# Kernel tuning notes

Hardware: AMD Instinct MI355X
Metric: run time of the kernel (lower is better)

Reference implementation:

```python
import jax, jax.numpy as jnp
import numpy as np

NEG_SLOPE = 0.2
EPS = 1e-5

N_NODES = 50000
N_GRAPHS = 500
NODES_PER_GRAPH = 100
N_EDGES = 500000
F_IN = 16
F_GRAPH = 4
HID = 64
N_CLASSES = 2


def setup_inputs() -> dict:
    key = jax.random.key(0)
    ks = jax.random.split(key, 32)
    x = jax.random.normal(ks[0], (N_NODES, F_IN), dtype=jnp.float32)
    # intra-graph random edges: dst lives in the same 100-node block as src
    src = jax.random.randint(ks[1], (N_EDGES,), 0, N_NODES)
    dst = (src // NODES_PER_GRAPH) * NODES_PER_GRAPH + jax.random.randint(ks[2], (N_EDGES,), 0, NODES_PER_GRAPH)
    edge_index = jnp.stack([src, dst]).astype(jnp.int64)
    graph_input = jax.random.normal(ks[3], (N_GRAPHS, F_GRAPH), dtype=jnp.float32)
    batch = (jnp.arange(N_NODES) // NODES_PER_GRAPH).astype(jnp.int64)

    def w(k, shape, scale=0.1):
        return (jax.random.normal(k, shape, dtype=jnp.float32) * scale)

    inp = dict(x=x, edge_index=edge_index, graph_input=graph_input, batch=batch)
    # GraphNorm params
    inp['gn_w'] = jnp.ones((F_IN,), jnp.float32)
    inp['gn_b'] = w(ks[4], (F_IN,))
    inp['gn_ms'] = jnp.ones((F_IN,), jnp.float32)
    inp['W1'] = w(ks[5], (F_IN, 4 * HID))
    inp['as1'] = w(ks[6], (4, HID)); inp['ad1'] = w(ks[7], (4, HID))
    inp['b1'] = w(ks[8], (4 * HID,))
    inp['W2'] = w(ks[9], (4 * HID, 4 * HID))
    inp['as2'] = w(ks[10], (4, HID)); inp['ad2'] = w(ks[11], (4, HID))
    inp['b2'] = w(ks[12], (4 * HID,))
    inp['W3'] = w(ks[13], (4 * HID, HID))
    inp['as3'] = w(ks[14], (1, HID)); inp['ad3'] = w(ks[15], (1, HID))
    inp['b3'] = w(ks[16], (HID,))
    # BatchNorm1d (eval mode) over [HID + F_GRAPH]
    D = HID + F_GRAPH
    inp['bn_g'] = 1.0 + w(ks[17], (D,))
    inp['bn_b'] = w(ks[18], (D,))
    inp['bn_m'] = jnp.zeros((D,), jnp.float32)
    inp['bn_v'] = jnp.ones((D,), jnp.float32)
    # Dense head
    inp['Wd1'] = w(ks[19], (D, HID)); inp['bd1'] = w(ks[20], (HID,))
    inp['Wd2'] = w(ks[21], (HID, HID)); inp['bd2'] = w(ks[22], (HID,))
    inp['Wo'] = w(ks[23], (HID, N_CLASSES)); inp['bo'] = w(ks[24], (N_CLASSES,))
    return inp


def _segment_softmax(e, seg, n):
    m = jax.ops.segment_max(e, seg, num_segments=n)
    ex = jnp.exp(e - m[seg])
    s = jax.ops.segment_sum(ex, seg, num_segments=n)
    return ex / s[seg]


def _gat_conv(x, src, dst, W, att_src, att_dst, b):
    N = x.shape[0]
    H, C = att_src.shape
    loop = jnp.arange(N)
    src = jnp.concatenate([src, loop])  # PyG GATConv adds self-loops
    dst = jnp.concatenate([dst, loop])
    h = (x @ W).reshape(N, H, C)
    a_src = (h * att_src).sum(-1)  # [N,H]
    a_dst = (h * att_dst).sum(-1)
    e = jax.nn.leaky_relu(a_src[src] + a_dst[dst], NEG_SLOPE)  # [E,H]
    alpha = _segment_softmax(e, dst, N)
    out = jax.ops.segment_sum(h[src] * alpha[:, :, None], dst, num_segments=N)
    return out.reshape(N, H * C) + b


def _graph_norm(x, batch, n_graphs, w, b, ms):
    cnt = jax.ops.segment_sum(jnp.ones((x.shape[0],), x.dtype), batch, num_segments=n_graphs)[:, None]
    mean = jax.ops.segment_sum(x, batch, num_segments=n_graphs) / cnt
    out = x - mean[batch] * ms
    var = jax.ops.segment_sum(out * out, batch, num_segments=n_graphs) / cnt
    return w * out / jnp.sqrt(var[batch] + EPS) + b


def _global_mean_pool(x, batch, n_graphs):
    cnt = jax.ops.segment_sum(jnp.ones((x.shape[0],), x.dtype), batch, num_segments=n_graphs)[:, None]
    return jax.ops.segment_sum(x, batch, num_segments=n_graphs) / cnt


def reference(x, edge_index, graph_input, batch,
              gn_w, gn_b, gn_ms,
              W1, as1, ad1, b1,
              W2, as2, ad2, b2,
              W3, as3, ad3, b3,
              bn_g, bn_b, bn_m, bn_v,
              Wd1, bd1, Wd2, bd2, Wo, bo):
    src, dst = edge_index[0], edge_index[1]
    G = graph_input.shape[0]
    h = _graph_norm(x, batch, G, gn_w, gn_b, gn_ms)
    # dropout is a no-op in eval
    h = jax.nn.elu(_gat_conv(h, src, dst, W1, as1, ad1, b1))
    h = jax.nn.elu(_gat_conv(h, src, dst, W2, as2, ad2, b2))
    h = _gat_conv(h, src, dst, W3, as3, ad3, b3)
    g = _global_mean_pool(h, batch, G)
    g = jnp.concatenate([g, graph_input], axis=1)
    g = (g - bn_m) / jnp.sqrt(bn_v + EPS) * bn_g + bn_b  # BatchNorm1d eval
    g = jax.nn.selu(g @ Wd1 + bd1)
    g = jax.nn.selu(g @ Wd2 + bd2)
    g = g @ Wo + bo
    return jax.nn.softmax(g, axis=1)
```

## Files before the change

kernel.cpp:

```cpp
#include <hip/hip_runtime.h>
#include <math.h>

#define N_NODES 50000
#define N_ROWS_PAD 50048
#define N_GRAPHS 500
#define NPG 100
#define N_EDGES 500000
#define F_IN 16
#define HID 64
#define EW_CAP 1408

#define SELU_SCALE 1.0507009873554804934193349852946f
#define SELU_ALPHA 1.6732632423543772848170429916717f

typedef __attribute__((ext_vector_type(8))) short short8;
typedef __attribute__((ext_vector_type(8))) unsigned short ushort8;
typedef __attribute__((ext_vector_type(4))) float floatx4;

__device__ __forceinline__ float lrelu(float x){ return x > 0.f ? x : 0.2f * x; }
__device__ __forceinline__ float eluf(float x){ return x > 0.f ? x : expf(x) - 1.f; }
__device__ __forceinline__ float seluf(float x){
    return x > 0.f ? SELU_SCALE * x : SELU_SCALE * (SELU_ALPHA * (expf(x) - 1.f));
}
__device__ __forceinline__ unsigned short f2bf(float x){
    unsigned u = __float_as_uint(x);
    return (unsigned short)((u + 0x7FFFu + ((u >> 16) & 1u)) >> 16);
}
__device__ __forceinline__ float bf2f(unsigned short u){
    return __uint_as_float((unsigned)u << 16);
}
__device__ __forceinline__ float bf2f_lo(unsigned u){
    return __uint_as_float(u << 16);
}
__device__ __forceinline__ float bf2f_hi(unsigned u){
    return __uint_as_float(u & 0xFFFF0000u);
}

__global__ void k_count(const int* __restrict__ dst, int* __restrict__ counts){
    int e = blockIdx.x * 256 + threadIdx.x;
    if (e < N_EDGES) atomicAdd(&counts[dst[e]], 1);
}

__global__ void k_local_scan(const int* __restrict__ counts, int* __restrict__ local_off,
                             int* __restrict__ graph_tot){
    __shared__ int s[128];
    int g = blockIdx.x, t = threadIdx.x;
    int v = (t < NPG) ? counts[g * NPG + t] : 0;
    s[t] = v; __syncthreads();
    for (int o = 1; o < 128; o <<= 1){
        int x = (t >= o) ? s[t - o] : 0;
        __syncthreads();
        s[t] += x;
        __syncthreads();
    }
    if (t < NPG) local_off[g * NPG + t] = s[t] - v;
    if (t == 127) graph_tot[g] = s[127];
}

__global__ void k_graph_scan(const int* __restrict__ graph_tot, int* __restrict__ graph_base){
    __shared__ int s[512];
    int t = threadIdx.x;
    int v = (t < N_GRAPHS) ? graph_tot[t] : 0;
    s[t] = v; __syncthreads();
    for (int o = 1; o < 512; o <<= 1){
        int x = (t >= o) ? s[t - o] : 0;
        __syncthreads();
        s[t] += x;
        __syncthreads();
    }
    if (t < N_GRAPHS) graph_base[t] = s[t] - v;
}

__global__ void k_off(const int* __restrict__ local_off, const int* __restrict__ graph_base,
                      int* __restrict__ node_off, int* __restrict__ write_ptr){
    int n = blockIdx.x * 256 + threadIdx.x;
    if (n < N_NODES){
        int v = local_off[n] + graph_base[n / NPG];
        node_off[n] = v;
        write_ptr[n] = v;
    }
}

__global__ void k_scatter(const int* __restrict__ src, const int* __restrict__ dst,
                          int* __restrict__ write_ptr, int* __restrict__ csr){
    int e = blockIdx.x * 256 + threadIdx.x;
    if (e < N_EDGES){
        int d = dst[e];
        int pos = atomicAdd(&write_ptr[d], 1);
        csr[pos] = src[e];
    }
}

__global__ void k_gnorm(const float* __restrict__ x, const float* __restrict__ w,
                        const float* __restrict__ b, const float* __restrict__ ms,
                        float* __restrict__ y){
    __shared__ float sx[NPG * F_IN];
    __shared__ float red[16][16];
    __shared__ float meanS[16], varS[16];
    int g = blockIdx.x, t = threadIdx.x;
    for (int idx = t; idx < NPG * F_IN; idx += 256) sx[idx] = x[g * NPG * F_IN + idx];
    __syncthreads();
    int f = t & 15, grp = t >> 4;
    float p = 0.f;
    for (int i = grp; i < NPG; i += 16) p += sx[i * 16 + f];
    red[grp][f] = p; __syncthreads();
    if (t < 16){
        float s = 0.f;
        for (int i = 0; i < 16; i++) s += red[i][t];
        meanS[t] = s * (1.f / 100.f);
    }
    __syncthreads();
    float mm = meanS[f] * ms[f];
    p = 0.f;
    for (int i = grp; i < NPG; i += 16){ float v = sx[i * 16 + f] - mm; p += v * v; }
    red[grp][f] = p; __syncthreads();
    if (t < 16){
        float s = 0.f;
        for (int i = 0; i < 16; i++) s += red[i][t];
        varS[t] = s * (1.f / 100.f);
    }
    __syncthreads();
    for (int idx = t; idx < NPG * F_IN; idx += 256){
        int ff = idx & 15;
        float v = sx[idx] - meanS[ff] * ms[ff];
        y[g * NPG * F_IN + idx] = w[ff] * v * rsqrtf(varS[ff] + 1e-5f) + b[ff];
    }
}

__global__ void k_gemm_tiled(const float* __restrict__ X, const float* __restrict__ W,
                             float* __restrict__ Y, int N, int K, int OUT){
    __shared__ float As[16][68];
    __shared__ float Bs[16][68];
    int t = threadIdx.x;
    int r0 = blockIdx.y * 64;
    int c0 = blockIdx.x * 64;
    int tx = t & 15, ty = t >> 4;
    float acc[4][4];
    #pragma unroll
    for (int i = 0; i < 4; i++)
        #pragma unroll
        for (int j = 0; j < 4; j++) acc[i][j] = 0.f;

    int lk = t & 15;
    int lm0 = t >> 4;
    int ln = t & 63;
    int lkb = t >> 6;

    for (int kt = 0; kt < K; kt += 16){
        #pragma unroll
        for (int i = 0; i < 4; i++){
            int m = lm0 + i * 16;
            int row = r0 + m;
            As[lk][m] = (row < N) ? X[row * K + kt + lk] : 0.f;
        }
        #pragma unroll
        for (int i = 0; i < 4; i++){
            int k = lkb + i * 4;
            Bs[k][ln] = W[(kt + k) * OUT + c0 + ln];
        }
        __syncthreads();
        #pragma unroll
        for (int k = 0; k < 16; k++){
            float4 a = *(const float4*)&As[k][ty * 4];
            float4 b = *(const float4*)&Bs[k][tx * 4];
            float av[4] = {a.x, a.y, a.z, a.w};
            float bv[4] = {b.x, b.y, b.z, b.w};
            #pragma unroll
            for (int i = 0; i < 4; i++)
                #pragma unroll
                for (int j = 0; j < 4; j++) acc[i][j] += av[i] * bv[j];
        }
        __syncthreads();
    }
    #pragma unroll
    for (int i = 0; i < 4; i++){
        int row = r0 + ty * 4 + i;
        if (row < N){
            float4 v = make_float4(acc[i][0], acc[i][1], acc[i][2], acc[i][3]);
            *(float4*)&Y[row * OUT + c0 + tx * 4] = v;
        }
    }
}

__global__ void k_pack_w(const float* __restrict__ W, unsigned short* __restrict__ Wp,
                         int K, int OUT){
    int idx = blockIdx.x * 256 + threadIdx.x;
    if (idx >= K * OUT) return;
    int k = idx / OUT, n = idx - k * OUT;
    Wp[(((k >> 3) * OUT) + n) * 8 + (k & 7)] = f2bf(W[idx]);
}

__global__ void k_gemm_mfma(const unsigned short* __restrict__ Xb,
                            const unsigned short* __restrict__ Wp,
                            float* __restrict__ Y, int N, int K, int OUT){
    int t = threadIdx.x;
    int wave = t >> 6, lane = t & 63;
    int quad = lane >> 4, ln = lane & 15;
    int r0 = blockIdx.y * 64 + wave * 16;
    int c0 = blockIdx.x * 64;

    floatx4 acc[4];
    #pragma unroll
    for (int f = 0; f < 4; f++) acc[f] = (floatx4){0.f, 0.f, 0.f, 0.f};

    const unsigned short* aptr = Xb + (size_t)(r0 + ln) * K + quad * 8;
    for (int kt = 0; kt < K; kt += 32){
        short8 a = *(const short8*)(aptr + kt);
        int kc = (kt >> 3) + quad;
        #pragma unroll
        for (int f = 0; f < 4; f++){
            short8 b = *(const short8*)(Wp + ((size_t)kc * OUT + c0 + f * 16 + ln) * 8);
            acc[f] = __builtin_amdgcn_mfma_f32_16x16x32_bf16(a, b, acc[f], 0, 0, 0);
        }
    }
    int rowb = r0 + quad * 4;
    #pragma unroll
    for (int f = 0; f < 4; f++){
        int col = c0 + f * 16 + ln;
        #pragma unroll
        for (int rg = 0; rg < 4; rg++){
            int row = rowb + rg;
            if (row < N) Y[(size_t)row * OUT + col] = acc[f][rg];
        }
    }
}

__global__ void __launch_bounds__(512)
k_fused4(const float* __restrict__ h, const float* __restrict__ as,
         const float* __restrict__ ad, const float* __restrict__ bias,
         const int* __restrict__ csr, const int* __restrict__ noff,
         const int* __restrict__ cnt, unsigned short* __restrict__ out_bf){
    __shared__ __align__(16) unsigned short hl[NPG * 256];
    __shared__ __align__(16) unsigned int edl[EW_CAP][4];
    __shared__ __align__(16) float asrcl[NPG * 4], adstl[NPG * 4];
    __shared__ __align__(16) float wselfl[NPG * 4], rsuml[NPG * 4];
    __shared__ int offl[NPG], cntl[NPG];

    int g = blockIdx.x, t = threadIdx.x;
    int wave = t >> 6, lane = t & 63;
    int base = g * NPG;

    int ebeg = noff[base];
    int etot = noff[base + NPG - 1] + cnt[base + NPG - 1] - ebeg;
    int eln = etot < EW_CAP ? etot : EW_CAP;

    for (int i = t; i < NPG * 16; i += 512){
        int node = i >> 4, c4 = i & 15;
        const float* hr = h + (size_t)(base + node) * 256 + c4 * 4;
        float4 f0 = *(const float4*)(hr);
        float4 f1 = *(const float4*)(hr + 64);
        float4 f2 = *(const float4*)(hr + 128);
        float4 f3 = *(const float4*)(hr + 192);
        ushort8 lo, hi;
        lo[0] = f2bf(f0.x); lo[1] = f2bf(f1.x); lo[2] = f2bf(f2.x); lo[3] = f2bf(f3.x);
        lo[4] = f2bf(f0.y); lo[5] = f2bf(f1.y); lo[6] = f2bf(f2.y); lo[7] = f2bf(f3.y);
        hi[0] = f2bf(f0.z); hi[1] = f2bf(f1.z); hi[2] = f2bf(f2.z); hi[3] = f2bf(f3.z);
        hi[4] = f2bf(f0.w); hi[5] = f2bf(f1.w); hi[6] = f2bf(f2.w); hi[7] = f2bf(f3.w);
        *(ushort8*)&hl[node * 256 + c4 * 16]     = lo;
        *(ushort8*)&hl[node * 256 + c4 * 16 + 8] = hi;
    }
    for (int i = t; i < eln; i += 512) edl[i][2] = (unsigned)(csr[ebeg + i] - base);
    if (t < NPG){ offl[t] = noff[base + t]; cntl[t] = cnt[base + t]; }
    __syncthreads();

    {
        int cl = lane & 15, nsub = lane >> 4;
        float av[4][4], dv[4][4];
        #pragma unroll
        for (int hh = 0; hh < 4; hh++){
            float4 a4 = *(const float4*)&as[hh * 64 + cl * 4];
            float4 d4 = *(const float4*)&ad[hh * 64 + cl * 4];
            av[hh][0] = a4.x; av[hh][1] = a4.y; av[hh][2] = a4.z; av[hh][3] = a4.w;
            dv[hh][0] = d4.x; dv[hh][1] = d4.y; dv[hh][2] = d4.z; dv[hh][3] = d4.w;
        }
        for (int g0 = wave * 4; g0 < NPG; g0 += 32){
            int n = g0 + nsub;
            ushort8 lo = *(const ushort8*)&hl[n * 256 + cl * 16];
            ushort8 hi = *(const ushort8*)&hl[n * 256 + cl * 16 + 8];
            float ps[4] = {0.f, 0.f, 0.f, 0.f}, pd[4] = {0.f, 0.f, 0.f, 0.f};
            #pragma unroll
            for (int k = 0; k < 2; k++){
                #pragma unroll
                for (int hh = 0; hh < 4; hh++){
                    float x = bf2f(lo[k * 4 + hh]);
                    ps[hh] = fmaf(x, av[hh][k], ps[hh]);
                    pd[hh] = fmaf(x, dv[hh][k], pd[hh]);
                }
            }
            #pragma unroll
            for (int k = 0; k < 2; k++){
                #pragma unroll
                for (int hh = 0; hh < 4; hh++){
                    float x = bf2f(hi[k * 4 + hh]);
                    ps[hh] = fmaf(x, av[hh][k + 2], ps[hh]);
                    pd[hh] = fmaf(x, dv[hh][k + 2], pd[hh]);
                }
            }
            #pragma unroll
            for (int o = 8; o >= 1; o >>= 1){
                #pragma unroll
                for (int hh = 0; hh < 4; hh++){
                    ps[hh] += __shfl_xor(ps[hh], o);
                    pd[hh] += __shfl_xor(pd[hh], o);
                }
            }
            if (cl == 0){
                *(float4*)&asrcl[n * 4] = make_float4(ps[0], ps[1], ps[2], ps[3]);
                *(float4*)&adstl[n * 4] = make_float4(pd[0], pd[1], pd[2], pd[3]);
            }
        }
    }
    __syncthreads();

    if (t < NPG * 4){
        int d = t >> 2, hh = t & 3;
        float adv = adstl[d * 4 + hh];
        float wsf = expf(lrelu(asrcl[d * 4 + hh] + adv));
        float sum = wsf;
        int ebg = offl[d] - ebeg, n = cntl[d];
        for (int j = 0; j < n; j++){
            int s = (int)edl[ebg + j][2];
            unsigned short u = f2bf(expf(lrelu(asrcl[s * 4 + hh] + adv)));
            ((unsigned short*)&edl[ebg + j][0])[hh] = u;
            sum += bf2f(u);
        }
        wselfl[d * 4 + hh] = wsf;
        rsuml[d * 4 + hh] = 1.f / sum;
    }
    __syncthreads();

    float b0 = bias[lane], b1 = bias[64 + lane], b2 = bias[128 + lane], b3 = bias[192 + lane];
    for (int d = wave; d < NPG; d += 8){
        float4 ws = *(const float4*)&wselfl[d * 4];
        float4 rs = *(const float4*)&rsuml[d * 4];
        ushort4 hv = *(const ushort4*)&hl[d * 256 + lane * 4];
        float a0 = ws.x * bf2f(hv.x);
        float a1 = ws.y * bf2f(hv.y);
        float a2 = ws.z * bf2f(hv.z);
        float a3 = ws.w * bf2f(hv.w);
        int ebg = offl[d] - ebeg, n = cntl[d];
        int j = 0;
        #pragma unroll 1
        for (; j + 4 <= n; j += 4){
            #pragma unroll
            for (int k = 0; k < 4; k++){
                uint4 v = *(const uint4*)&edl[ebg + j + k][0];
                int s = (int)v.z;
                ushort4 x = *(const ushort4*)&hl[s * 256 + lane * 4];
                a0 = fmaf(bf2f_lo(v.x), bf2f(x.x), a0);
                a1 = fmaf(bf2f_hi(v.x), bf2f(x.y), a1);
                a2 = fmaf(bf2f_lo(v.y), bf2f(x.z), a2);
                a3 = fmaf(bf2f_hi(v.y), bf2f(x.w), a3);
            }
        }
        for (; j < n; j++){
            uint4 v = *(const uint4*)&edl[ebg + j][0];
            int s = (int)v.z;
            ushort4 x = *(const ushort4*)&hl[s * 256 + lane * 4];
            a0 = fmaf(bf2f_lo(v.x), bf2f(x.x), a0);
            a1 = fmaf(bf2f_hi(v.x), bf2f(x.y), a1);
            a2 = fmaf(bf2f_lo(v.y), bf2f(x.z), a2);
            a3 = fmaf(bf2f_hi(v.y), bf2f(x.w), a3);
        }
        size_t ob = (size_t)(base + d) * 256 + lane;
        out_bf[ob]       = f2bf(eluf(a0 * rs.x + b0));
        out_bf[ob + 64]  = f2bf(eluf(a1 * rs.y + b1));
        out_bf[ob + 128] = f2bf(eluf(a2 * rs.z + b2));
        out_bf[ob + 192] = f2bf(eluf(a3 * rs.w + b3));
    }
}

__global__ void __launch_bounds__(256)
k_fused1(const float* __restrict__ h, const float* __restrict__ as,
         const float* __restrict__ ad, const float* __restrict__ bias,
         const int* __restrict__ csr, const int* __restrict__ noff,
         const int* __restrict__ cnt, float* __restrict__ out){
    __shared__ __align__(16) unsigned short hl[NPG * 64];
    __shared__ __align__(16) unsigned int edl[EW_CAP][2];
    __shared__ float asrcl[NPG], adstl[NPG];
    __shared__ float wselfl[NPG], rsuml[NPG];
    __shared__ int offl[NPG], cntl[NPG];

    int g = blockIdx.x, t = threadIdx.x;
    int wave = t >> 6, lane = t & 63;
    int base = g * NPG;

    int ebeg = noff[base];
    int etot = noff[base + NPG - 1] + cnt[base + NPG - 1] - ebeg;
    int eln = etot < EW_CAP ? etot : EW_CAP;

    const float4* hsrc = (const float4*)(h + (size_t)base * 64);
    for (int i = t; i < NPG * 8; i += 256){
        float4 v0 = hsrc[i * 2];
        float4 v1 = hsrc[i * 2 + 1];
        ushort8 u;
        u[0] = f2bf(v0.x); u[1] = f2bf(v0.y); u[2] = f2bf(v0.z); u[3] = f2bf(v0.w);
        u[4] = f2bf(v1.x); u[5] = f2bf(v1.y); u[6] = f2bf(v1.z); u[7] = f2bf(v1.w);
        *(ushort8*)&hl[i * 8] = u;
    }
    for (int i = t; i < eln; i += 256) edl[i][1] = (unsigned)(csr[ebeg + i] - base);
    if (t < NPG){ offl[t] = noff[base + t]; cntl[t] = cnt[base + t]; }
    __syncthreads();

    {
        int cl = lane & 15, nsub = lane >> 4;
        float4 a4 = *(const float4*)&as[cl * 4];
        float4 d4 = *(const float4*)&ad[cl * 4];
        for (int g0 = wave * 4; g0 < NPG; g0 += 16){
            int n = g0 + nsub;
            ushort4 u = *(const ushort4*)&hl[n * 64 + cl * 4];
            float x0 = bf2f(u.x), x1 = bf2f(u.y), x2 = bf2f(u.z), x3 = bf2f(u.w);
            float ps = x0 * a4.x + x1 * a4.y + x2 * a4.z + x3 * a4.w;
            float pd = x0 * d4.x + x1 * d4.y + x2 * d4.z + x3 * d4.w;
            #pragma unroll
            for (int o = 8; o >= 1; o >>= 1){
                ps += __shfl_xor(ps, o);
                pd += __shfl_xor(pd, o);
            }
            if (cl == 0){ asrcl[n] = ps; adstl[n] = pd; }
        }
    }
    __syncthreads();

    if (t < NPG){
        float adv = adstl[t];
        float wsf = expf(lrelu(asrcl[t] + adv));
        float sum = wsf;
        int ebg = offl[t] - ebeg, n = cntl[t];
        for (int j = 0; j < n; j++){
            int s = (int)edl[ebg + j][1];
            unsigned short u = f2bf(expf(lrelu(asrcl[s] + adv)));
            edl[ebg + j][0] = (unsigned)u;
            sum += bf2f(u);
        }
        wselfl[t] = wsf;
        rsuml[t] = 1.f / sum;
    }
    __syncthreads();

    float bl = bias[lane];
    for (int d = wave; d < NPG; d += 4){
        float acc = wselfl[d] * bf2f(hl[d * 64 + lane]);
        int ebg = offl[d] - ebeg, n = cntl[d];
        for (int j = 0; j < n; j++){
            uint2 v = *(const uint2*)&edl[ebg + j][0];
            acc = fmaf(bf2f_lo(v.x), bf2f(hl[(int)v.y * 64 + lane]), acc);
        }
        out[(size_t)(base + d) * 64 + lane] = acc * rsuml[d] + bl;
    }
}

__global__ void k_head(const float* __restrict__ x3, const float* __restrict__ gin,
                       const float* __restrict__ bn_g, const float* __restrict__ bn_b,
                       const float* __restrict__ bn_m, const float* __restrict__ bn_v,
                       const float* __restrict__ Wd1, const float* __restrict__ bd1,
                       const float* __restrict__ Wd2, const float* __restrict__ bd2,
                       const float* __restrict__ Wo, const float* __restrict__ bo,
                       float* __restrict__ out){
    __shared__ float red[256];
    __shared__ float gv[68];
    __shared__ float g2[64];
    __shared__ float g3[64];
    int g = blockIdx.x, t = threadIdx.x;
    int c = t & 63, grp = t >> 6;
    float p = 0.f;
    for (int i = grp; i < NPG; i += 4) p += x3[(g * NPG + i) * 64 + c];
    red[t] = p; __syncthreads();
    if (t < 64){
        float s = red[t] + red[t + 64] + red[t + 128] + red[t + 192];
        float mean = s * (1.f / 100.f);
        gv[t] = (mean - bn_m[t]) * rsqrtf(bn_v[t] + 1e-5f) * bn_g[t] + bn_b[t];
    } else if (t < 68){
        int j = t - 64;
        float v = gin[g * 4 + j];
        gv[t] = (v - bn_m[t]) * rsqrtf(bn_v[t] + 1e-5f) * bn_g[t] + bn_b[t];
    }
    __syncthreads();
    if (t < 64){
        float s = bd1[t];
        for (int i = 0; i < 68; i++) s += gv[i] * Wd1[i * 64 + t];
        g2[t] = seluf(s);
    }
    __syncthreads();
    if (t < 64){
        float s = bd2[t];
        for (int i = 0; i < 64; i++) s += g2[i] * Wd2[i * 64 + t];
        g3[t] = seluf(s);
    }
    __syncthreads();
    if (t == 0){
        float l0 = bo[0], l1 = bo[1];
        for (int i = 0; i < 64; i++){ l0 += g3[i] * Wo[i * 2]; l1 += g3[i] * Wo[i * 2 + 1]; }
        float mx = fmaxf(l0, l1);
        float e0 = expf(l0 - mx), e1 = expf(l1 - mx);
        float inv = 1.f / (e0 + e1);
        out[g * 2] = e0 * inv;
        out[g * 2 + 1] = e1 * inv;
    }
}

extern "C" void kernel_launch(void* const* d_in, const int* in_sizes, int n_in,
                              void* d_out, int out_size, void* d_ws, size_t ws_size,
                              hipStream_t stream){
    const float* x   = (const float*)d_in[0];
    const int*   ei  = (const int*)d_in[1];
    const float* gin = (const float*)d_in[2];
    const float* gn_w = (const float*)d_in[4];
    const float* gn_b = (const float*)d_in[5];
    const float* gn_ms = (const float*)d_in[6];
    const float* W1 = (const float*)d_in[7];
    const float* as1 = (const float*)d_in[8];
    const float* ad1 = (const float*)d_in[9];
    const float* b1 = (const float*)d_in[10];
    const float* W2 = (const float*)d_in[11];
    const float* as2 = (const float*)d_in[12];
    const float* ad2 = (const float*)d_in[13];
    const float* b2 = (const float*)d_in[14];
    const float* W3 = (const float*)d_in[15];
    const float* as3 = (const float*)d_in[16];
    const float* ad3 = (const float*)d_in[17];
    const float* b3 = (const float*)d_in[18];
    const float* bn_g = (const float*)d_in[19];
    const float* bn_b = (const float*)d_in[20];
    const float* bn_m = (const float*)d_in[21];
    const float* bn_v = (const float*)d_in[22];
    const float* Wd1 = (const float*)d_in[23];
    const float* bd1 = (const float*)d_in[24];
    const float* Wd2 = (const float*)d_in[25];
    const float* bd2 = (const float*)d_in[26];
    const float* Wo = (const float*)d_in[27];
    const float* bo = (const float*)d_in[28];
    float* out = (float*)d_out;

    const int* src = ei;
    const int* dst = ei + N_EDGES;

    char* ws = (char*)d_ws;
    size_t off = 0;
    auto alloc = [&](size_t bytes) -> void* {
        void* p = ws + off;
        off = (off + bytes + 255) & ~(size_t)255;
        return p;
    };
    int* counts     = (int*)alloc((size_t)N_NODES * 4);
    int* local_off  = (int*)alloc((size_t)N_NODES * 4);
    int* node_off   = (int*)alloc((size_t)N_NODES * 4);
    int* write_ptr  = (int*)alloc((size_t)N_NODES * 4);
    int* graph_tot  = (int*)alloc(512 * 4);
    int* graph_base = (int*)alloc(512 * 4);
    int* csr        = (int*)alloc((size_t)N_EDGES * 4);
    float* y        = (float*)alloc((size_t)N_NODES * F_IN * 4);
    unsigned short* wp2 = (unsigned short*)alloc((size_t)256 * 256 * 2);
    unsigned short* wp3 = (unsigned short*)alloc((size_t)256 * 64 * 2);
    float* bufA     = (float*)alloc((size_t)N_NODES * 256 * 4);
    unsigned short* xb = (unsigned short*)alloc((size_t)N_ROWS_PAD * 256 * 2);
    float* bufC     = (float*)alloc((size_t)N_NODES * HID * 4);
    float* bufD     = (float*)alloc((size_t)N_NODES * HID * 4);

    hipMemsetAsync(counts, 0, (size_t)N_NODES * 4, stream);
    k_count<<<(N_EDGES + 255) / 256, 256, 0, stream>>>(dst, counts);
    k_local_scan<<<N_GRAPHS, 128, 0, stream>>>(counts, local_off, graph_tot);
    k_graph_scan<<<1, 512, 0, stream>>>(graph_tot, graph_base);
    k_off<<<(N_NODES + 255) / 256, 256, 0, stream>>>(local_off, graph_base, node_off, write_ptr);
    k_scatter<<<(N_EDGES + 255) / 256, 256, 0, stream>>>(src, dst, write_ptr, csr);

    k_pack_w<<<(256 * 256 + 255) / 256, 256, 0, stream>>>(W2, wp2, 256, 256);
    k_pack_w<<<(256 * 64 + 255) / 256, 256, 0, stream>>>(W3, wp3, 256, 64);

    k_gnorm<<<N_GRAPHS, 256, 0, stream>>>(x, gn_w, gn_b, gn_ms, y);

    dim3 gemm_grid4(4, (N_NODES + 63) / 64);
    dim3 mfma_grid4(4, N_ROWS_PAD / 64);
    dim3 mfma_grid1(1, N_ROWS_PAD / 64);

    k_gemm_tiled<<<gemm_grid4, 256, 0, stream>>>(y, W1, bufA, N_NODES, 16, 256);
    k_fused4<<<N_GRAPHS, 512, 0, stream>>>(bufA, as1, ad1, b1, csr, node_off, counts, xb);

    k_gemm_mfma<<<mfma_grid4, 256, 0, stream>>>(xb, wp2, bufA, N_NODES, 256, 256);
    k_fused4<<<N_GRAPHS, 512, 0, stream>>>(bufA, as2, ad2, b2, csr, node_off, counts, xb);

    k_gemm_mfma<<<mfma_grid1, 256, 0, stream>>>(xb, wp3, bufC, N_NODES, 256, 64);
    k_fused1<<<N_GRAPHS, 256, 0, stream>>>(bufC, as3, ad3, b3, csr, node_off, counts, bufD);

    k_head<<<N_GRAPHS, 256, 0, stream>>>(bufD, gin, bn_g, bn_b, bn_m, bn_v,
                                         Wd1, bd1, Wd2, bd2, Wo, bo, out);
}
```

Before: 351.7 us.

## Emit bf16 head-interleaved GEMM outputs and parallelize edge attention weights per edge

The GEMM kernels now write bf16 directly in the head-interleaved layout the GAT aggregation kernels expect, so the fused kernels just copy rows into shared memory instead of loading fp32 and converting. This halves the intermediate feature traffic. The CSR entries now pack local source and destination indices, so attention weights are computed in parallel per edge rather than serially per destination node. Only the row sums remain per node. Writing interleaved bf16 from the GEMMs uses scattered 2-byte stores, which may hurt store coalescing.

```diff
diff --git a/kernel.cpp b/kernel.cpp
--- a/kernel.cpp
+++ b/kernel.cpp
@@ -87,7 +87,8 @@
     if (e < N_EDGES){
         int d = dst[e];
         int pos = atomicAdd(&write_ptr[d], 1);
-        csr[pos] = src[e];
+        int b = (d / NPG) * NPG;
+        csr[pos] = (src[e] - b) | ((d - b) << 8);
     }
 }
 
@@ -128,7 +129,7 @@
 }
 
 __global__ void k_gemm_tiled(const float* __restrict__ X, const float* __restrict__ W,
-                             float* __restrict__ Y, int N, int K, int OUT){
+                             unsigned short* __restrict__ Ybf, int N, int K, int OUT){
     __shared__ float As[16][68];
     __shared__ float Bs[16][68];
     int t = threadIdx.x;
@@ -172,12 +173,14 @@
         }
         __syncthreads();
     }
+    int hh = c0 >> 6;
     #pragma unroll
     for (int i = 0; i < 4; i++){
         int row = r0 + ty * 4 + i;
         if (row < N){
-            float4 v = make_float4(acc[i][0], acc[i][1], acc[i][2], acc[i][3]);
-            *(float4*)&Y[row * OUT + c0 + tx * 4] = v;
+            #pragma unroll
+            for (int j = 0; j < 4; j++)
+                Ybf[(size_t)row * 256 + (tx * 4 + j) * 4 + hh] = f2bf(acc[i][j]);
         }
     }
 }
@@ -192,7 +195,8 @@
 
 __global__ void k_gemm_mfma(const unsigned short* __restrict__ Xb,
                             const unsigned short* __restrict__ Wp,
-                            float* __restrict__ Y, int N, int K, int OUT){
+                            unsigned short* __restrict__ Ybf,
+                            int N, int K, int OUT, int interleave){
     int t = threadIdx.x;
     int wave = t >> 6, lane = t & 63;
     int quad = lane >> 4, ln = lane & 15;
@@ -214,19 +218,32 @@
         }
     }
     int rowb = r0 + quad * 4;
-    #pragma unroll
-    for (int f = 0; f < 4; f++){
-        int col = c0 + f * 16 + ln;
-        #pragma unroll
-        for (int rg = 0; rg < 4; rg++){
-            int row = rowb + rg;
-            if (row < N) Y[(size_t)row * OUT + col] = acc[f][rg];
+    if (interleave){
+        int hh = c0 >> 6;
+        #pragma unroll
+        for (int f = 0; f < 4; f++){
+            int c = f * 16 + ln;
+            #pragma unroll
+            for (int rg = 0; rg < 4; rg++){
+                int row = rowb + rg;
+                if (row < N) Ybf[(size_t)row * 256 + c * 4 + hh] = f2bf(acc[f][rg]);
+            }
+        }
+    } else {
+        #pragma unroll
+        for (int f = 0; f < 4; f++){
+            int col = c0 + f * 16 + ln;
+            #pragma unroll
+            for (int rg = 0; rg < 4; rg++){
+                int row = rowb + rg;
+                if (row < N) Ybf[(size_t)row * OUT + col] = f2bf(acc[f][rg]);
+            }
         }
     }
 }
 
 __global__ void __launch_bounds__(512)
-k_fused4(const float* __restrict__ h, const float* __restrict__ as,
+k_fused4(const unsigned short* __restrict__ hbf, const float* __restrict__ as,
          const float* __restrict__ ad, const float* __restrict__ bias,
          const int* __restrict__ csr, const int* __restrict__ noff,
          const int* __restrict__ cnt, unsigned short* __restrict__ out_bf){
@@ -244,22 +261,9 @@
     int etot = noff[base + NPG - 1] + cnt[base + NPG - 1] - ebeg;
     int eln = etot < EW_CAP ? etot : EW_CAP;
 
-    for (int i = t; i < NPG * 16; i += 512){
-        int node = i >> 4, c4 = i & 15;
-        const float* hr = h + (size_t)(base + node) * 256 + c4 * 4;
-        float4 f0 = *(const float4*)(hr);
-        float4 f1 = *(const float4*)(hr + 64);
-        float4 f2 = *(const float4*)(hr + 128);
-        float4 f3 = *(const float4*)(hr + 192);
-        ushort8 lo, hi;
-        lo[0] = f2bf(f0.x); lo[1] = f2bf(f1.x); lo[2] = f2bf(f2.x); lo[3] = f2bf(f3.x);
-        lo[4] = f2bf(f0.y); lo[5] = f2bf(f1.y); lo[6] = f2bf(f2.y); lo[7] = f2bf(f3.y);
-        hi[0] = f2bf(f0.z); hi[1] = f2bf(f1.z); hi[2] = f2bf(f2.z); hi[3] = f2bf(f3.z);
-        hi[4] = f2bf(f0.w); hi[5] = f2bf(f1.w); hi[6] = f2bf(f2.w); hi[7] = f2bf(f3.w);
-        *(ushort8*)&hl[node * 256 + c4 * 16]     = lo;
-        *(ushort8*)&hl[node * 256 + c4 * 16 + 8] = hi;
-    }
-    for (int i = t; i < eln; i += 512) edl[i][2] = (unsigned)(csr[ebeg + i] - base);
+    const ushort8* hsrc = (const ushort8*)(hbf + (size_t)base * 256);
+    for (int i = t; i < NPG * 32; i += 512) ((ushort8*)hl)[i] = hsrc[i];
+    for (int i = t; i < eln; i += 512) edl[i][2] = (unsigned)csr[ebeg + i];
     if (t < NPG){ offl[t] = noff[base + t]; cntl[t] = cnt[base + t]; }
     __syncthreads();
 
@@ -312,20 +316,37 @@
     }
     __syncthreads();
 
-    if (t < NPG * 4){
-        int d = t >> 2, hh = t & 3;
-        float adv = adstl[d * 4 + hh];
-        float wsf = expf(lrelu(asrcl[d * 4 + hh] + adv));
-        float sum = wsf;
+    for (int i = t; i < eln; i += 512){
+        unsigned sd = edl[i][2];
+        int s = sd & 0xFF, d = sd >> 8;
+        float4 av = *(const float4*)&asrcl[s * 4];
+        float4 dv = *(const float4*)&adstl[d * 4];
+        unsigned w0 = f2bf(expf(lrelu(av.x + dv.x)));
+        unsigned w1 = f2bf(expf(lrelu(av.y + dv.y)));
+        unsigned w2 = f2bf(expf(lrelu(av.z + dv.z)));
+        unsigned w3 = f2bf(expf(lrelu(av.w + dv.w)));
+        edl[i][0] = w0 | (w1 << 16);
+        edl[i][1] = w2 | (w3 << 16);
+    }
+    __syncthreads();
+
+    if (t < NPG){
+        int d = t;
+        float4 av = *(const float4*)&asrcl[d * 4];
+        float4 dv = *(const float4*)&adstl[d * 4];
+        float ws0 = expf(lrelu(av.x + dv.x));
+        float ws1 = expf(lrelu(av.y + dv.y));
+        float ws2 = expf(lrelu(av.z + dv.z));
+        float ws3 = expf(lrelu(av.w + dv.w));
+        float s0 = ws0, s1 = ws1, s2 = ws2, s3 = ws3;
         int ebg = offl[d] - ebeg, n = cntl[d];
         for (int j = 0; j < n; j++){
-            int s = (int)edl[ebg + j][2];
-            unsigned short u = f2bf(expf(lrelu(asrcl[s * 4 + hh] + adv)));
-            ((unsigned short*)&edl[ebg + j][0])[hh] = u;
-            sum += bf2f(u);
-        }
-        wselfl[d * 4 + hh] = wsf;
-        rsuml[d * 4 + hh] = 1.f / sum;
+            uint2 v = *(const uint2*)&edl[ebg + j][0];
+            s0 += bf2f_lo(v.x); s1 += bf2f_hi(v.x);
+            s2 += bf2f_lo(v.y); s3 += bf2f_hi(v.y);
+        }
+        *(float4*)&wselfl[d * 4] = make_float4(ws0, ws1, ws2, ws3);
+        *(float4*)&rsuml[d * 4]  = make_float4(1.f / s0, 1.f / s1, 1.f / s2, 1.f / s3);
     }
     __syncthreads();
 
@@ -345,7 +366,7 @@
             #pragma unroll
             for (int k = 0; k < 4; k++){
                 uint4 v = *(const uint4*)&edl[ebg + j + k][0];
-                int s = (int)v.z;
+                int s = (int)(v.z & 0xFFu);
                 ushort4 x = *(const ushort4*)&hl[s * 256 + lane * 4];
                 a0 = fmaf(bf2f_lo(v.x), bf2f(x.x), a0);
                 a1 = fmaf(bf2f_hi(v.x), bf2f(x.y), a1);
@@ -355,7 +376,7 @@
         }
         for (; j < n; j++){
             uint4 v = *(const uint4*)&edl[ebg + j][0];
-            int s = (int)v.z;
+            int s = (int)(v.z & 0xFFu);
             ushort4 x = *(const ushort4*)&hl[s * 256 + lane * 4];
             a0 = fmaf(bf2f_lo(v.x), bf2f(x.x), a0);
             a1 = fmaf(bf2f_hi(v.x), bf2f(x.y), a1);
@@ -371,7 +392,7 @@
 }
 
 __global__ void __launch_bounds__(256)
-k_fused1(const float* __restrict__ h, const float* __restrict__ as,
+k_fused1(const unsigned short* __restrict__ hbf, const float* __restrict__ as,
          const float* __restrict__ ad, const float* __restrict__ bias,
          const int* __restrict__ csr, const int* __restrict__ noff,
          const int* __restrict__ cnt, float* __restrict__ out){
@@ -389,16 +410,9 @@
     int etot = noff[base + NPG - 1] + cnt[base + NPG - 1] - ebeg;
     int eln = etot < EW_CAP ? etot : EW_CAP;
 
-    const float4* hsrc = (const float4*)(h + (size_t)base * 64);
-    for (int i = t; i < NPG * 8; i += 256){
-        float4 v0 = hsrc[i * 2];
-        float4 v1 = hsrc[i * 2 + 1];
-        ushort8 u;
-        u[0] = f2bf(v0.x); u[1] = f2bf(v0.y); u[2] = f2bf(v0.z); u[3] = f2bf(v0.w);
-        u[4] = f2bf(v1.x); u[5] = f2bf(v1.y); u[6] = f2bf(v1.z); u[7] = f2bf(v1.w);
-        *(ushort8*)&hl[i * 8] = u;
-    }
-    for (int i = t; i < eln; i += 256) edl[i][1] = (unsigned)(csr[ebeg + i] - base);
+    const ushort8* hsrc = (const ushort8*)(hbf + (size_t)base * 64);
+    for (int i = t; i < NPG * 8; i += 256) ((ushort8*)hl)[i] = hsrc[i];
+    for (int i = t; i < eln; i += 256) edl[i][1] = (unsigned)csr[ebeg + i];
     if (t < NPG){ offl[t] = noff[base + t]; cntl[t] = cnt[base + t]; }
     __syncthreads();
 
@@ -422,17 +436,18 @@
     }
     __syncthreads();
 
+    for (int i = t; i < eln; i += 256){
+        unsigned sd = edl[i][1];
+        int s = sd & 0xFF, d = sd >> 8;
+        edl[i][0] = (unsigned)f2bf(expf(lrelu(asrcl[s] + adstl[d])));
+    }
+    __syncthreads();
+
     if (t < NPG){
-        float adv = adstl[t];
-        float wsf = expf(lrelu(asrcl[t] + adv));
+        float wsf = expf(lrelu(asrcl[t] + adstl[t]));
         float sum = wsf;
         int ebg = offl[t] - ebeg, n = cntl[t];
-        for (int j = 0; j < n; j++){
-            int s = (int)edl[ebg + j][1];
-            unsigned short u = f2bf(expf(lrelu(asrcl[s] + adv)));
-            edl[ebg + j][0] = (unsigned)u;
-            sum += bf2f(u);
-        }
+        for (int j = 0; j < n; j++) sum += bf2f((unsigned short)edl[ebg + j][0]);
         wselfl[t] = wsf;
         rsuml[t] = 1.f / sum;
     }
@@ -444,7 +459,7 @@
         int ebg = offl[d] - ebeg, n = cntl[d];
         for (int j = 0; j < n; j++){
             uint2 v = *(const uint2*)&edl[ebg + j][0];
-            acc = fmaf(bf2f_lo(v.x), bf2f(hl[(int)v.y * 64 + lane]), acc);
+            acc = fmaf(bf2f_lo(v.x), bf2f(hl[(int)(v.y & 0xFFu) * 64 + lane]), acc);
         }
         out[(size_t)(base + d) * 64 + lane] = acc * rsuml[d] + bl;
     }
@@ -552,9 +567,9 @@
     float* y        = (float*)alloc((size_t)N_NODES * F_IN * 4);
     unsigned short* wp2 = (unsigned short*)alloc((size_t)256 * 256 * 2);
     unsigned short* wp3 = (unsigned short*)alloc((size_t)256 * 64 * 2);
-    float* bufA     = (float*)alloc((size_t)N_NODES * 256 * 4);
-    unsigned short* xb = (unsigned short*)alloc((size_t)N_ROWS_PAD * 256 * 2);
-    float* bufC     = (float*)alloc((size_t)N_NODES * HID * 4);
+    unsigned short* xbh = (unsigned short*)alloc((size_t)N_NODES * 256 * 2);
+    unsigned short* xb  = (unsigned short*)alloc((size_t)N_ROWS_PAD * 256 * 2);
+    unsigned short* x3b = (unsigned short*)alloc((size_t)N_NODES * HID * 2);
     float* bufD     = (float*)alloc((size_t)N_NODES * HID * 4);
 
     hipMemsetAsync(counts, 0, (size_t)N_NODES * 4, stream);
@@ -573,14 +588,14 @@
     dim3 mfma_grid4(4, N_ROWS_PAD / 64);
     dim3 mfma_grid1(1, N_ROWS_PAD / 64);
 
-    k_gemm_tiled<<<gemm_grid4, 256, 0, stream>>>(y, W1, bufA, N_NODES, 16, 256);
-    k_fused4<<<N_GRAPHS, 512, 0, stream>>>(bufA, as1, ad1, b1, csr, node_off, counts, xb);
-
-    k_gemm_mfma<<<mfma_grid4, 256, 0, stream>>>(xb, wp2, bufA, N_NODES, 256, 256);
-    k_fused4<<<N_GRAPHS, 512, 0, stream>>>(bufA, as2, ad2, b2, csr, node_off, counts, xb);
-
-    k_gemm_mfma<<<mfma_grid1, 256, 0, stream>>>(xb, wp3, bufC, N_NODES, 256, 64);
-    k_fused1<<<N_GRAPHS, 256, 0, stream>>>(bufC, as3, ad3, b3, csr, node_off, counts, bufD);
+    k_gemm_tiled<<<gemm_grid4, 256, 0, stream>>>(y, W1, xbh, N_NODES, 16, 256);
+    k_fused4<<<N_GRAPHS, 512, 0, stream>>>(xbh, as1, ad1, b1, csr, node_off, counts, xb);
+
+    k_gemm_mfma<<<mfma_grid4, 256, 0, stream>>>(xb, wp2, xbh, N_NODES, 256, 256, 1);
+    k_fused4<<<N_GRAPHS, 512, 0, stream>>>(xbh, as2, ad2, b2, csr, node_off, counts, xb);
+
+    k_gemm_mfma<<<mfma_grid1, 256, 0, stream>>>(xb, wp3, x3b, N_NODES, 256, 64, 0);
+    k_fused1<<<N_GRAPHS, 256, 0, stream>>>(x3b, as3, ad3, b3, csr, node_off, counts, bufD);
 
     k_head<<<N_GRAPHS, 256, 0, stream>>>(bufD, gin, bn_g, bn_b, bn_m, bn_v,
                                          Wd1, bd1, Wd2, bd2, Wo, bo, out);
```

After: 381.7 us. 1.09x slower.
